# Kernel tuning notes

Hardware: AMD Instinct MI355X
Metric: run time of the kernel (lower is better)

Reference implementation:

```python
import jax, jax.numpy as jnp
import numpy as np

# Config constants (match init_kwargs)
E = 16          # n_routed_experts
G = 4           # n_groups
TOPK_G = 2      # topk_groups
K = 4           # n_activated_experts
ROUTE_SCALE = 2.5446


def setup_inputs() -> dict:
    key = jax.random.key(0)
    ks = jax.random.split(key, 9)
    T, D, H = 2048, 1024, 704
    HS = 2 * H  # shared FFN hidden = n_shared_experts * expert_hidden_dim
    sc = lambda k, shape, fan_in: (jax.random.normal(k, shape, jnp.float32)
                                   * (fan_in ** -0.5))
    return {
        "x":      jax.random.normal(ks[0], (T, D), jnp.float32),
        "gate_w": sc(ks[1], (E, D), D),
        "gate_b": jnp.zeros((E,), jnp.float32),       # V3 routing bias (init 0)
        "w1":     sc(ks[2], (E, H, D), D),            # gate proj per expert
        "w3":     sc(ks[3], (E, H, D), D),            # up proj per expert
        "w2":     sc(ks[4], (E, D, H), H),            # down proj per expert
        "ws1":    sc(ks[5], (HS, D), D),              # shared FFN gate proj
        "ws3":    sc(ks[6], (HS, D), D),              # shared FFN up proj
        "ws2":    sc(ks[7], (D, HS), HS),             # shared FFN down proj
    }


def _gate(x, gate_w, gate_b):
    """DeepSeek-V3 sigmoid gate with bias routing + group-limited masking."""
    T = x.shape[0]
    logits = x @ gate_w.T                                   # [T, E]
    scores = jax.nn.sigmoid(logits).astype(jnp.float32)     # original_scores
    routing = scores + gate_b                               # bias only affects routing
    g = routing.reshape(T, G, E // G)
    # use_bias=True -> group score = sum of top-2 routing scores in group
    group_scores = jnp.sum(jax.lax.top_k(g, 2)[0], axis=-1)     # [T, G]
    top_groups = jax.lax.top_k(group_scores, TOPK_G)[1]         # [T, TOPK_G]
    keep = jnp.any(jnp.arange(G)[None, :, None] == top_groups[:, None, :],
                   axis=-1)                                     # [T, G]
    routing = jnp.where(keep[:, :, None], g, -jnp.inf).reshape(T, E)
    idx = jax.lax.top_k(routing, K)[1]                          # [T, K]
    w = jnp.take_along_axis(scores, idx, axis=1)                # un-biased weights
    w = w / jnp.clip(jnp.sum(w, axis=-1, keepdims=True), 1e-9)  # sigmoid renorm
    w = (w * ROUTE_SCALE).astype(x.dtype)
    return w, idx


def reference(x, gate_w, gate_b, w1, w3, w2, ws1, ws3, ws2):
    T, D = x.shape
    weights, idx = _gate(x, gate_w, gate_b)                 # [T,K], [T,K]
    # Dense dispatch/combine matrix: combine[t, e] = gate weight (0 if unrouted)
    combine = jnp.zeros((T, E), x.dtype).at[
        jnp.arange(T)[:, None], idx].add(weights)           # [T, E]
    # Routed experts: SwiGLU per expert, grouped GEMMs
    hg = jnp.einsum('td,ehd->eth', x, w1)                   # [E, T, H]
    hu = jnp.einsum('td,ehd->eth', x, w3)                   # [E, T, H]
    eo = jnp.einsum('eth,edh->etd', jax.nn.silu(hg) * hu, w2)  # [E, T, D]
    y_routed = jnp.einsum('etd,te->td', eo, combine)        # [T, D]
    # Shared experts (always active SwiGLU)
    y_shared = (jax.nn.silu(x @ ws1.T) * (x @ ws3.T)) @ ws2.T
    return y_routed + y_shared
```

## Files before the change

kernel.cpp:

```cpp
#include <hip/hip_runtime.h>
#include <hip/hip_bf16.h>
#include <math.h>

typedef __attribute__((ext_vector_type(4))) float   f32x4;
typedef __attribute__((ext_vector_type(8))) short   short8;
typedef __attribute__((ext_vector_type(8))) __bf16  bf16x8;

union SB8 { short8 s; bf16x8 b; };

__device__ __forceinline__ short f2bf(float f) {
  union { float f; unsigned u; } v; v.f = f;
  unsigned r = v.u + 0x7fffu + ((v.u >> 16) & 1u);
  return (short)(r >> 16);
}

__device__ __forceinline__ short8 cvt8(f32x4 a, f32x4 b) {
  short8 r;
  r[0] = f2bf(a[0]); r[1] = f2bf(a[1]); r[2] = f2bf(a[2]); r[3] = f2bf(a[3]);
  r[4] = f2bf(b[0]); r[5] = f2bf(b[1]); r[6] = f2bf(b[2]); r[7] = f2bf(b[3]);
  return r;
}

__device__ __forceinline__ void ldsload16(const short* g, short* l) {
  __builtin_amdgcn_global_load_lds(
      (const __attribute__((address_space(1))) unsigned int*)g,
      (__attribute__((address_space(3))) unsigned int*)l, 16, 0, 0);
}

#define TT   2048
#define DD   1024
#define HH   704
#define HSS  1408
#define EE   16
#define CAP  2048
#define CSTR 32
#define XSZ  2097152ULL
#define GATE_BLOCKS 512
#define XCVT_BLOCKS 256

__global__ __launch_bounds__(256)
void gate_cvt(const float* __restrict__ x, short* __restrict__ xb,
              const float* __restrict__ gw, const float* __restrict__ gb,
              int* __restrict__ counts, int* __restrict__ tok,
              float* __restrict__ wgt, int* __restrict__ eslot)
{
  if (blockIdx.x >= GATE_BLOCKS) {
    const int tid = threadIdx.x;
    const size_t base = (size_t)(blockIdx.x - GATE_BLOCKS) * 8192;
    f32x4 va[8];
    #pragma unroll
    for (int k = 0; k < 4; k++) {
      va[2 * k]     = *(const f32x4*)(x + base + (size_t)k * 2048 + tid * 8);
      va[2 * k + 1] = *(const f32x4*)(x + base + (size_t)k * 2048 + tid * 8 + 4);
    }
    #pragma unroll
    for (int k = 0; k < 4; k++)
      *(short8*)(xb + base + (size_t)k * 2048 + tid * 8) = cvt8(va[2 * k], va[2 * k + 1]);
    return;
  }

  const int lane = threadIdx.x & 63;
  const int wid  = threadIdx.x >> 6;
  const int t    = blockIdx.x * 4 + wid;
  const int e    = lane & 15;
  const int p    = lane >> 4;

  const float* xp = x + (size_t)t * DD + p * 256;
  const float* gp = gw + (size_t)e * DD + p * 256;

  double a0 = 0.0, a1 = 0.0, a2 = 0.0, a3 = 0.0;
  #pragma unroll 8
  for (int i = 0; i < 64; i++) {
    f32x4 xa = *(const f32x4*)(xp + i * 4);
    f32x4 ga = *(const f32x4*)(gp + i * 4);
    a0 += (double)xa[0] * (double)ga[0];
    a1 += (double)xa[1] * (double)ga[1];
    a2 += (double)xa[2] * (double)ga[2];
    a3 += (double)xa[3] * (double)ga[3];
  }
  double acc = (a0 + a1) + (a2 + a3);
  acc += __shfl_xor(acc, 16);
  acc += __shfl_xor(acc, 32);
  float accf = (float)acc;

  float lf[EE], sc[EE], r[EE];
  #pragma unroll
  for (int j = 0; j < EE; j++) lf[j] = __shfl(accf, j);
  #pragma unroll
  for (int j = 0; j < EE; j++) {
    sc[j] = 1.f / (1.f + expf(-lf[j]));
    r[j] = sc[j] + gb[j];
  }
  float gs[4];
  #pragma unroll
  for (int g = 0; g < 4; g++) {
    float m1 = -1e30f, m2 = -1e30f;
    #pragma unroll
    for (int j = 0; j < 4; j++) {
      float v = r[g * 4 + j];
      if (v > m1) { m2 = m1; m1 = v; }
      else if (v > m2) { m2 = v; }
    }
    gs[g] = m1 + m2;
  }
  int g1 = 0, g2 = -1; float b1 = -1e30f, b2 = -1e30f;
  #pragma unroll
  for (int g = 0; g < 4; g++) {
    if (gs[g] > b1) { b2 = b1; g2 = g1; b1 = gs[g]; g1 = g; }
    else if (gs[g] > b2) { b2 = gs[g]; g2 = g; }
  }
  int idx[4]; float wv[4]; float wsum = 0.f;
  unsigned used = 0;
  #pragma unroll
  for (int k = 0; k < 4; k++) {
    float best = -1e30f; int bi = 0;
    #pragma unroll
    for (int j = 0; j < EE; j++) {
      int g = j >> 2;
      bool keep = (g == g1) || (g == g2);
      if (keep && !((used >> j) & 1) && r[j] > best) { best = r[j]; bi = j; }
    }
    used |= 1u << bi; idx[k] = bi; wv[k] = sc[bi]; wsum += sc[bi];
  }
  float div = wsum < 1e-9f ? 1e-9f : wsum;
  if (lane < 4) {
    float w = wv[lane] / div * 2.5446f;
    int slot = atomicAdd(&counts[idx[lane] * CSTR], 1);
    tok[idx[lane] * CAP + slot] = t;
    wgt[idx[lane] * CAP + slot] = w;
    eslot[t * 4 + lane] = (idx[lane] << 16) | slot;
  }
}

#define PIPE_VM_WAIT() do { \
    asm volatile("s_waitcnt vmcnt(0)" ::: "memory"); \
    __builtin_amdgcn_sched_barrier(0); \
    __builtin_amdgcn_s_barrier(); \
    __builtin_amdgcn_sched_barrier(0); } while (0)
#define PIPE_LGKM_BAR() do { \
    asm volatile("s_waitcnt lgkmcnt(0)" ::: "memory"); \
    __builtin_amdgcn_sched_barrier(0); \
    __builtin_amdgcn_s_barrier(); \
    __builtin_amdgcn_sched_barrier(0); } while (0)

__global__ __launch_bounds__(512, 2)
void gemm1_merged(const short* __restrict__ xb,
                  const float* __restrict__ w1f, const float* __restrict__ w3f,
                  const float* __restrict__ ws1f, const float* __restrict__ ws3f,
                  short* __restrict__ act_r, short* __restrict__ act_s,
                  const int* __restrict__ counts, const int* __restrict__ tok)
{
  const int F = blockIdx.x + 11 * (blockIdx.y + 16 * blockIdx.z);
  const int r8 = F & 7, rank = F >> 3;
  int z, Mt, Ntc;
  if (rank < 352) {
    z = r8 + 8 * (rank / 176);
    const int p = rank % 176;
    Mt = p / 11; Ntc = p % 11;
  } else {
    z = 16;
    const int p = (rank - 352) * 8 + r8;
    Mt = p / 22; Ntc = p % 22;
  }

  const bool routed = (z < EE);
  int cnt, N, rowbase = 0;
  const float *W1, *W3;
  short* act;
  if (routed) {
    cnt = counts[z * CSTR];
    if (Mt * 128 >= cnt) return;
    int rb = 0;
    for (int i = 0; i < z; i++) rb += counts[i * CSTR];
    rowbase = rb;
    N = HH;
    W1 = w1f + (size_t)z * HH * DD;
    W3 = w3f + (size_t)z * HH * DD;
    act = act_r;
  } else {
    cnt = TT; N = HSS; W1 = ws1f; W3 = ws3f; act = act_s;
  }
  const int NtB = Ntc * 64;

  __shared__ __align__(16) short lA [2][128 * 64];
  __shared__ __align__(16) short lB1[2][64 * 64];
  __shared__ __align__(16) short lB3[2][64 * 64];

  const int tid = threadIdx.x, lane = tid & 63, wv = tid >> 6;
  const int srow = lane >> 3, schunk = lane & 7, scg = schunk ^ srow;

  const short* pa[2];
  #pragma unroll
  for (int i = 0; i < 2; i++) {
    const int g = wv * 2 + i;
    int arow = Mt * 128 + g * 8 + srow;
    if (routed) {
      int slot = arow < cnt ? arow : cnt - 1;
      arow = tok[z * CAP + slot];
    }
    pa[i] = xb + (size_t)arow * DD + scg * 8;
  }
  const float *pb1f, *pb3f;
  {
    const int brow = NtB + wv * 8 + srow;
    pb1f = W1 + (size_t)brow * DD + scg * 8;
    pb3f = W3 + (size_t)brow * DD + scg * 8;
  }

  f32x4 acc1[4], acc3[4];
  #pragma unroll
  for (int i = 0; i < 4; i++) { acc1[i] = (f32x4)0.f; acc3[i] = (f32x4)0.f; }
  f32x4 rb1[2], rb3[2];

  const int q = lane >> 4, r7 = lane & 7, hi = (lane & 15) >> 3;
  const int wc = wv & 3, mh = wv >> 2;
  const int wofs = wv * 512 + srow * 64 + schunk * 8;

#define STAGE1_ISSUE(c, kk) do { \
    ldsload16(pa[0] + (kk), &lA[c][(wv * 2 + 0) * 512]); \
    ldsload16(pa[1] + (kk), &lA[c][(wv * 2 + 1) * 512]); \
    rb1[0] = *(const f32x4*)(pb1f + (kk)); \
    rb1[1] = *(const f32x4*)(pb1f + (kk) + 4); \
    rb3[0] = *(const f32x4*)(pb3f + (kk)); \
    rb3[1] = *(const f32x4*)(pb3f + (kk) + 4); } while (0)

#define STAGE1_WRITE(c) do { \
    *(short8*)(&lB1[c][wofs]) = cvt8(rb1[0], rb1[1]); \
    *(short8*)(&lB3[c][wofs]) = cvt8(rb3[0], rb3[1]); } while (0)

#define GEMM1_BODY(c) do { \
    _Pragma("unroll") for (int kc = 0; kc < 2; kc++) { \
      const int cx = (kc * 4 + q) ^ r7; \
      SB8 b1f, b3f; \
      b1f.s = *(const short8*)(&lB1[c][((wc * 2 + hi) * 64 + r7 * 8 + cx) * 8]); \
      b3f.s = *(const short8*)(&lB3[c][((wc * 2 + hi) * 64 + r7 * 8 + cx) * 8]); \
      _Pragma("unroll") for (int mt = 0; mt < 4; mt++) { \
        SB8 af; af.s = *(const short8*)(&lA[c][((2 * (mh * 4 + mt) + hi) * 64 + r7 * 8 + cx) * 8]); \
        acc1[mt] = __builtin_amdgcn_mfma_f32_16x16x32_bf16(af.b, b1f.b, acc1[mt], 0, 0, 0); \
        acc3[mt] = __builtin_amdgcn_mfma_f32_16x16x32_bf16(af.b, b3f.b, acc3[mt], 0, 0, 0); \
      } } } while (0)

  STAGE1_ISSUE(0, 0);
  asm volatile("s_waitcnt vmcnt(0)" ::: "memory");
  __builtin_amdgcn_sched_barrier(0);
  STAGE1_WRITE(0);
  PIPE_LGKM_BAR();
  int cur = 0;
  for (int kk = 64; kk < DD; kk += 64) {
    STAGE1_ISSUE(cur ^ 1, kk);
    GEMM1_BODY(cur);
    PIPE_VM_WAIT();
    STAGE1_WRITE(cur ^ 1);
    PIPE_LGKM_BAR();
    cur ^= 1;
  }
  GEMM1_BODY(cur);

  const int quad = lane >> 4, lcol = lane & 15;
  const int col = NtB + wc * 16 + lcol;
  #pragma unroll
  for (int mt = 0; mt < 4; mt++) {
    #pragma unroll
    for (int rg = 0; rg < 4; rg++) {
      const int r = Mt * 128 + (mh * 4 + mt) * 16 + quad * 4 + rg;
      if (r < cnt) {
        float g = acc1[mt][rg], u = acc3[mt][rg];
        float a = g / (1.f + __expf(-g)) * u;
        act[(size_t)(rowbase + r) * N + col] = f2bf(a);
      }
    }
  }
#undef STAGE1_ISSUE
#undef STAGE1_WRITE
#undef GEMM1_BODY
}

__global__ __launch_bounds__(512, 2)
void gemm2_merged(const short* __restrict__ act_r, const short* __restrict__ act_s,
                  const float* __restrict__ w2f, const float* __restrict__ ws2f,
                  float* __restrict__ y, float* __restrict__ outr,
                  const int* __restrict__ counts, const float* __restrict__ wgt)
{
  const int F = blockIdx.x + 8 * (blockIdx.y + 16 * blockIdx.z);
  const int r8 = F & 7, rank = F >> 3;
  int z, Mt, Nt;
  if (rank < 256) {
    z = r8 + 8 * (rank >> 7);
    const int p = rank & 127;
    Mt = p >> 3; Nt = p & 7;
  } else {
    z = 16;
    const int p = (rank - 256) * 8 + r8;
    Mt = p >> 3; Nt = p & 7;
  }

  const bool routed = (z < EE);

  int cnt, Kd, rowbase = 0;
  const short* A;
  const float* W;
  if (routed) {
    cnt = counts[z * CSTR];
    if (Mt * 128 >= cnt) return;
    int rb = 0;
    for (int i = 0; i < z; i++) rb += counts[i * CSTR];
    rowbase = rb;
    Kd = HH;
    A = act_r + (size_t)rowbase * HH;
    W = w2f + (size_t)z * DD * HH;
  } else {
    cnt = TT; Kd = HSS; A = act_s; W = ws2f;
  }

  __shared__ __align__(16) short lA[2][128 * 64];
  __shared__ __align__(16) short lB[2][128 * 64];

  const int tid = threadIdx.x, lane = tid & 63, wv = tid >> 6;
  const int srow = lane >> 3, schunk = lane & 7, scg = schunk ^ srow;

  const short* pa[2]; const float* pbf[2];
  #pragma unroll
  for (int i = 0; i < 2; i++) {
    const int g = wv * 2 + i;
    int arow = Mt * 128 + g * 8 + srow;
    if (arow >= cnt) arow = cnt - 1;
    pa[i] = A + (size_t)arow * Kd + scg * 8;
    const int brow = Nt * 128 + g * 8 + srow;
    pbf[i] = W + (size_t)brow * Kd + scg * 8;
  }

  f32x4 acc[4][2];
  #pragma unroll
  for (int i = 0; i < 4; i++) { acc[i][0] = (f32x4)0.f; acc[i][1] = (f32x4)0.f; }
  f32x4 rbw[4];

  const int q = lane >> 4, r7 = lane & 7, hi = (lane & 15) >> 3;
  const int wc = wv & 3, mh = wv >> 2;
  const int wofs0 = (wv * 2 + 0) * 512 + srow * 64 + schunk * 8;
  const int wofs1 = (wv * 2 + 1) * 512 + srow * 64 + schunk * 8;

#define STAGE2_ISSUE(c, kk) do { \
    ldsload16(pa[0] + (kk), &lA[c][(wv * 2 + 0) * 512]); \
    ldsload16(pa[1] + (kk), &lA[c][(wv * 2 + 1) * 512]); \
    rbw[0] = *(const f32x4*)(pbf[0] + (kk)); \
    rbw[1] = *(const f32x4*)(pbf[0] + (kk) + 4); \
    rbw[2] = *(const f32x4*)(pbf[1] + (kk)); \
    rbw[3] = *(const f32x4*)(pbf[1] + (kk) + 4); } while (0)

#define STAGE2_WRITE(c) do { \
    *(short8*)(&lB[c][wofs0]) = cvt8(rbw[0], rbw[1]); \
    *(short8*)(&lB[c][wofs1]) = cvt8(rbw[2], rbw[3]); } while (0)

#define GEMM2_BODY(c) do { \
    _Pragma("unroll") for (int kc = 0; kc < 2; kc++) { \
      const int cx = (kc * 4 + q) ^ r7; \
      SB8 bf[2]; \
      _Pragma("unroll") for (int ntl = 0; ntl < 2; ntl++) { \
        const int a16 = ((wc * 2 + ntl) * 2 + hi) * 64 + r7 * 8 + cx; \
        bf[ntl].s = *(const short8*)(&lB[c][a16 * 8]); \
      } \
      _Pragma("unroll") for (int mt = 0; mt < 4; mt++) { \
        const int a16 = (2 * (mh * 4 + mt) + hi) * 64 + r7 * 8 + cx; \
        SB8 af; af.s = *(const short8*)(&lA[c][a16 * 8]); \
        acc[mt][0] = __builtin_amdgcn_mfma_f32_16x16x32_bf16(af.b, bf[0].b, acc[mt][0], 0, 0, 0); \
        acc[mt][1] = __builtin_amdgcn_mfma_f32_16x16x32_bf16(af.b, bf[1].b, acc[mt][1], 0, 0, 0); \
      } } } while (0)

  STAGE2_ISSUE(0, 0);
  asm volatile("s_waitcnt vmcnt(0)" ::: "memory");
  __builtin_amdgcn_sched_barrier(0);
  STAGE2_WRITE(0);
  PIPE_LGKM_BAR();
  int cur = 0;
  for (int kk = 64; kk < Kd; kk += 64) {
    STAGE2_ISSUE(cur ^ 1, kk);
    GEMM2_BODY(cur);
    PIPE_VM_WAIT();
    STAGE2_WRITE(cur ^ 1);
    PIPE_LGKM_BAR();
    cur ^= 1;
  }
  GEMM2_BODY(cur);

  const int quad = lane >> 4, lcol = lane & 15;
  #pragma unroll
  for (int mt = 0; mt < 4; mt++) {
    #pragma unroll
    for (int ntl = 0; ntl < 2; ntl++) {
      const int col = Nt * 128 + (wc * 2 + ntl) * 16 + lcol;
      #pragma unroll
      for (int rg = 0; rg < 4; rg++) {
        const int slot = Mt * 128 + (mh * 4 + mt) * 16 + quad * 4 + rg;
        const float v = acc[mt][ntl][rg];
        if (routed) {
          if (slot < cnt) {
            const float w = wgt[z * CAP + slot];
            outr[(size_t)(rowbase + slot) * DD + col] = w * v;
          }
        } else {
          y[(size_t)slot * DD + col] = v;
        }
      }
    }
  }
#undef STAGE2_ISSUE
#undef STAGE2_WRITE
#undef GEMM2_BODY
}

__global__ __launch_bounds__(256)
void combine_kernel(float* __restrict__ y, const float* __restrict__ outr,
                    const int* __restrict__ eslot, const int* __restrict__ counts)
{
  const int t = blockIdx.x;
  const int d = threadIdx.x * 4;

  int offs[EE];
  int s = 0;
  #pragma unroll
  for (int i = 0; i < EE; i++) { offs[i] = s; s += counts[i * CSTR]; }

  f32x4 accv = *(f32x4*)(y + (size_t)t * DD + d);
  #pragma unroll
  for (int k = 0; k < 4; k++) {
    const int es = eslot[t * 4 + k];
    const int row = offs[es >> 16] + (es & 0xFFFF);
    accv += *(const f32x4*)(outr + (size_t)row * DD + d);
  }
  *(f32x4*)(y + (size_t)t * DD + d) = accv;
}

extern "C" void kernel_launch(void* const* d_in, const int* in_sizes, int n_in,
                              void* d_out, int out_size, void* d_ws, size_t ws_size,
                              hipStream_t stream) {
  const float* x      = (const float*)d_in[0];
  const float* gate_w = (const float*)d_in[1];
  const float* gate_b = (const float*)d_in[2];
  const float* w1     = (const float*)d_in[3];
  const float* w3     = (const float*)d_in[4];
  const float* w2     = (const float*)d_in[5];
  const float* ws1    = (const float*)d_in[6];
  const float* ws3    = (const float*)d_in[7];
  const float* ws2    = (const float*)d_in[8];
  float* y = (float*)d_out;

  char* ws = (char*)d_ws;
  int*   counts = (int*)ws;
  int*   tok    = (int*)(ws + 2048);
  float* wgt    = (float*)(ws + 2048 + (size_t)EE * CAP * 4);
  int*   eslot  = (int*)(ws + 2048 + (size_t)EE * CAP * 8);
  short* xb     = (short*)(ws + 2048 + (size_t)EE * CAP * 8 + (size_t)TT * 16);
  short* act_r  = xb + XSZ;
  short* act_s  = act_r + (size_t)8192 * HH;
  float* outr   = (float*)(act_s + (size_t)TT * HSS);

  (void)hipMemsetAsync(counts, 0, EE * CSTR * sizeof(int), stream);

  gate_cvt<<<GATE_BLOCKS + XCVT_BLOCKS, 256, 0, stream>>>(
      x, xb, gate_w, gate_b, counts, tok, wgt, eslot);

  gemm1_merged<<<dim3(11, TT / 128, EE + 2), 512, 0, stream>>>(
      xb, w1, w3, ws1, ws3, act_r, act_s, counts, tok);

  gemm2_merged<<<dim3(DD / 128, TT / 128, EE + 1), 512, 0, stream>>>(
      act_r, act_s, w2, ws2, y, outr, counts, wgt);

  combine_kernel<<<TT, 256, 0, stream>>>(y, outr, eslot, counts);
}
```

Measured before the change: 347.8 us.

## Pre-convert gate/up weights to bf16 and scatter outputs with atomics

The conversion kernel now turns w1, w3, ws1 and ws3 to bf16 in one bulk pass alongside x. The first GEMM can then stream all operands with direct global-to-LDS loads, using a vmcnt-based double-buffer wait in place of the register convert-and-store path. The second GEMM atomically adds weighted results straight into a zeroed y, which removes the outr buffer and the combine kernel. The cost is an extra full read and write of the weights each call, many float atomics, and a summation order that is no longer fixed.

```diff
diff --git a/kernel.cpp b/kernel.cpp
--- a/kernel.cpp
+++ b/kernel.cpp
@@ -34,28 +34,48 @@
 #define EE   16
 #define CAP  2048
 #define CSTR 32
-#define XSZ  2097152ULL
+
+#define O1  2097152ULL
+#define O2  13631488ULL
+#define O3  25165824ULL
+#define WS1END 26607616ULL
+#define CVTA_TOTAL 28049408ULL
+#define CVTA_BLOCKS 3424
 #define GATE_BLOCKS 512
-#define XCVT_BLOCKS 256
 
 __global__ __launch_bounds__(256)
-void gate_cvt(const float* __restrict__ x, short* __restrict__ xb,
+void gate_cvt(const float* __restrict__ x,  const float* __restrict__ w1,
+              const float* __restrict__ w3, const float* __restrict__ s1,
+              const float* __restrict__ s3, short* __restrict__ dst,
               const float* __restrict__ gw, const float* __restrict__ gb,
               int* __restrict__ counts, int* __restrict__ tok,
-              float* __restrict__ wgt, int* __restrict__ eslot)
+              float* __restrict__ wgt)
 {
   if (blockIdx.x >= GATE_BLOCKS) {
     const int tid = threadIdx.x;
     const size_t base = (size_t)(blockIdx.x - GATE_BLOCKS) * 8192;
+    const float* sp[4]; short* dp[4];
+    #pragma unroll
+    for (int k = 0; k < 4; k++) {
+      const size_t sb = base + (size_t)k * 2048;
+      const float* src;
+      if      (sb < O1)     src = x  + sb;
+      else if (sb < O2)     src = w1 + (sb - O1);
+      else if (sb < O3)     src = w3 + (sb - O2);
+      else if (sb < WS1END) src = s1 + (sb - O3);
+      else                  src = s3 + (sb - WS1END);
+      sp[k] = src + tid * 8;
+      dp[k] = dst + sb + tid * 8;
+    }
     f32x4 va[8];
     #pragma unroll
     for (int k = 0; k < 4; k++) {
-      va[2 * k]     = *(const f32x4*)(x + base + (size_t)k * 2048 + tid * 8);
-      va[2 * k + 1] = *(const f32x4*)(x + base + (size_t)k * 2048 + tid * 8 + 4);
+      va[2 * k]     = *(const f32x4*)(sp[k]);
+      va[2 * k + 1] = *(const f32x4*)(sp[k] + 4);
     }
     #pragma unroll
     for (int k = 0; k < 4; k++)
-      *(short8*)(xb + base + (size_t)k * 2048 + tid * 8) = cvt8(va[2 * k], va[2 * k + 1]);
+      *(short8*)(dp[k]) = cvt8(va[2 * k], va[2 * k + 1]);
     return;
   }
 
@@ -128,10 +148,22 @@
     int slot = atomicAdd(&counts[idx[lane] * CSTR], 1);
     tok[idx[lane] * CAP + slot] = t;
     wgt[idx[lane] * CAP + slot] = w;
-    eslot[t * 4 + lane] = (idx[lane] << 16) | slot;
-  }
-}
-
+  }
+}
+
+#define WAIT_PREV_TILE()  do { \
+    asm volatile("s_waitcnt vmcnt(4)" ::: "memory"); \
+    __builtin_amdgcn_sched_barrier(0); \
+    __builtin_amdgcn_s_barrier(); \
+    __builtin_amdgcn_sched_barrier(0); } while (0)
+#define WAIT_LAST_TILE()  do { \
+    asm volatile("s_waitcnt vmcnt(0)" ::: "memory"); \
+    __builtin_amdgcn_sched_barrier(0); \
+    __builtin_amdgcn_s_barrier(); \
+    __builtin_amdgcn_sched_barrier(0); } while (0)
+#define END_TILE_BARRIER() do { \
+    __builtin_amdgcn_sched_barrier(0); \
+    __builtin_amdgcn_s_barrier(); } while (0)
 #define PIPE_VM_WAIT() do { \
     asm volatile("s_waitcnt vmcnt(0)" ::: "memory"); \
     __builtin_amdgcn_sched_barrier(0); \
@@ -144,11 +176,11 @@
     __builtin_amdgcn_sched_barrier(0); } while (0)
 
 __global__ __launch_bounds__(512, 2)
-void gemm1_merged(const short* __restrict__ xb,
-                  const float* __restrict__ w1f, const float* __restrict__ w3f,
-                  const float* __restrict__ ws1f, const float* __restrict__ ws3f,
-                  short* __restrict__ act_r, short* __restrict__ act_s,
-                  const int* __restrict__ counts, const int* __restrict__ tok)
+void gemm1_merged(const short* __restrict__ xb, const short* __restrict__ w1b,
+                  const short* __restrict__ w3b, const short* __restrict__ ws1b,
+                  const short* __restrict__ ws3b, short* __restrict__ act_r,
+                  short* __restrict__ act_s, const int* __restrict__ counts,
+                  const int* __restrict__ tok)
 {
   const int F = blockIdx.x + 11 * (blockIdx.y + 16 * blockIdx.z);
   const int r8 = F & 7, rank = F >> 3;
@@ -165,7 +197,7 @@
 
   const bool routed = (z < EE);
   int cnt, N, rowbase = 0;
-  const float *W1, *W3;
+  const short *W1, *W3;
   short* act;
   if (routed) {
     cnt = counts[z * CSTR];
@@ -174,11 +206,11 @@
     for (int i = 0; i < z; i++) rb += counts[i * CSTR];
     rowbase = rb;
     N = HH;
-    W1 = w1f + (size_t)z * HH * DD;
-    W3 = w3f + (size_t)z * HH * DD;
+    W1 = w1b + (size_t)z * HH * DD;
+    W3 = w3b + (size_t)z * HH * DD;
     act = act_r;
   } else {
-    cnt = TT; N = HSS; W1 = ws1f; W3 = ws3f; act = act_s;
+    cnt = TT; N = HSS; W1 = ws1b; W3 = ws3b; act = act_s;
   }
   const int NtB = Ntc * 64;
 
@@ -200,33 +232,25 @@
     }
     pa[i] = xb + (size_t)arow * DD + scg * 8;
   }
-  const float *pb1f, *pb3f;
+  const short *pb1, *pb3;
   {
     const int brow = NtB + wv * 8 + srow;
-    pb1f = W1 + (size_t)brow * DD + scg * 8;
-    pb3f = W3 + (size_t)brow * DD + scg * 8;
+    pb1 = W1 + (size_t)brow * DD + scg * 8;
+    pb3 = W3 + (size_t)brow * DD + scg * 8;
   }
 
   f32x4 acc1[4], acc3[4];
   #pragma unroll
   for (int i = 0; i < 4; i++) { acc1[i] = (f32x4)0.f; acc3[i] = (f32x4)0.f; }
-  f32x4 rb1[2], rb3[2];
 
   const int q = lane >> 4, r7 = lane & 7, hi = (lane & 15) >> 3;
   const int wc = wv & 3, mh = wv >> 2;
-  const int wofs = wv * 512 + srow * 64 + schunk * 8;
-
-#define STAGE1_ISSUE(c, kk) do { \
-    ldsload16(pa[0] + (kk), &lA[c][(wv * 2 + 0) * 512]); \
-    ldsload16(pa[1] + (kk), &lA[c][(wv * 2 + 1) * 512]); \
-    rb1[0] = *(const f32x4*)(pb1f + (kk)); \
-    rb1[1] = *(const f32x4*)(pb1f + (kk) + 4); \
-    rb3[0] = *(const f32x4*)(pb3f + (kk)); \
-    rb3[1] = *(const f32x4*)(pb3f + (kk) + 4); } while (0)
-
-#define STAGE1_WRITE(c) do { \
-    *(short8*)(&lB1[c][wofs]) = cvt8(rb1[0], rb1[1]); \
-    *(short8*)(&lB3[c][wofs]) = cvt8(rb3[0], rb3[1]); } while (0)
+
+#define STAGE1(c, kk) do { \
+    ldsload16(pa[0] + (kk), &lA [c][(wv * 2 + 0) * 512]); \
+    ldsload16(pa[1] + (kk), &lA [c][(wv * 2 + 1) * 512]); \
+    ldsload16(pb1  + (kk),  &lB1[c][wv * 512]); \
+    ldsload16(pb3  + (kk),  &lB3[c][wv * 512]); } while (0)
 
 #define GEMM1_BODY(c) do { \
     _Pragma("unroll") for (int kc = 0; kc < 2; kc++) { \
@@ -240,20 +264,16 @@
         acc3[mt] = __builtin_amdgcn_mfma_f32_16x16x32_bf16(af.b, b3f.b, acc3[mt], 0, 0, 0); \
       } } } while (0)
 
-  STAGE1_ISSUE(0, 0);
-  asm volatile("s_waitcnt vmcnt(0)" ::: "memory");
-  __builtin_amdgcn_sched_barrier(0);
-  STAGE1_WRITE(0);
-  PIPE_LGKM_BAR();
+  STAGE1(0, 0);
   int cur = 0;
   for (int kk = 64; kk < DD; kk += 64) {
-    STAGE1_ISSUE(cur ^ 1, kk);
+    STAGE1(cur ^ 1, kk);
+    WAIT_PREV_TILE();
     GEMM1_BODY(cur);
-    PIPE_VM_WAIT();
-    STAGE1_WRITE(cur ^ 1);
-    PIPE_LGKM_BAR();
+    END_TILE_BARRIER();
     cur ^= 1;
   }
+  WAIT_LAST_TILE();
   GEMM1_BODY(cur);
 
   const int quad = lane >> 4, lcol = lane & 15;
@@ -270,16 +290,16 @@
       }
     }
   }
-#undef STAGE1_ISSUE
-#undef STAGE1_WRITE
+#undef STAGE1
 #undef GEMM1_BODY
 }
 
 __global__ __launch_bounds__(512, 2)
 void gemm2_merged(const short* __restrict__ act_r, const short* __restrict__ act_s,
                   const float* __restrict__ w2f, const float* __restrict__ ws2f,
-                  float* __restrict__ y, float* __restrict__ outr,
-                  const int* __restrict__ counts, const float* __restrict__ wgt)
+                  float* __restrict__ y,
+                  const int* __restrict__ counts, const float* __restrict__ wgt,
+                  const int* __restrict__ tok)
 {
   const int F = blockIdx.x + 8 * (blockIdx.y + 16 * blockIdx.z);
   const int r8 = F & 7, rank = F >> 3;
@@ -395,10 +415,11 @@
         if (routed) {
           if (slot < cnt) {
             const float w = wgt[z * CAP + slot];
-            outr[(size_t)(rowbase + slot) * DD + col] = w * v;
+            const int t = tok[z * CAP + slot];
+            atomicAdd(&y[(size_t)t * DD + col], w * v);
           }
         } else {
-          y[(size_t)slot * DD + col] = v;
+          atomicAdd(&y[(size_t)slot * DD + col], v);
         }
       }
     }
@@ -406,28 +427,6 @@
 #undef STAGE2_ISSUE
 #undef STAGE2_WRITE
 #undef GEMM2_BODY
-}
-
-__global__ __launch_bounds__(256)
-void combine_kernel(float* __restrict__ y, const float* __restrict__ outr,
-                    const int* __restrict__ eslot, const int* __restrict__ counts)
-{
-  const int t = blockIdx.x;
-  const int d = threadIdx.x * 4;
-
-  int offs[EE];
-  int s = 0;
-  #pragma unroll
-  for (int i = 0; i < EE; i++) { offs[i] = s; s += counts[i * CSTR]; }
-
-  f32x4 accv = *(f32x4*)(y + (size_t)t * DD + d);
-  #pragma unroll
-  for (int k = 0; k < 4; k++) {
-    const int es = eslot[t * 4 + k];
-    const int row = offs[es >> 16] + (es & 0xFFFF);
-    accv += *(const f32x4*)(outr + (size_t)row * DD + d);
-  }
-  *(f32x4*)(y + (size_t)t * DD + d) = accv;
 }
 
 extern "C" void kernel_launch(void* const* d_in, const int* in_sizes, int n_in,
@@ -448,22 +447,25 @@
   int*   counts = (int*)ws;
   int*   tok    = (int*)(ws + 2048);
   float* wgt    = (float*)(ws + 2048 + (size_t)EE * CAP * 4);
-  int*   eslot  = (int*)(ws + 2048 + (size_t)EE * CAP * 8);
-  short* xb     = (short*)(ws + 2048 + (size_t)EE * CAP * 8 + (size_t)TT * 16);
-  short* act_r  = xb + XSZ;
-  short* act_s  = act_r + (size_t)8192 * HH;
-  float* outr   = (float*)(act_s + (size_t)TT * HSS);
+  short* bf     = (short*)(ws + 2048 + (size_t)EE * CAP * 8);
+  short* xb   = bf;
+  short* w1b  = bf + O1;
+  short* w3b  = bf + O2;
+  short* ws1b = bf + O3;
+  short* ws3b = bf + WS1END;
+  short* act_r = bf + CVTA_TOTAL;
+  short* act_s = act_r + (size_t)8192 * HH;
 
   (void)hipMemsetAsync(counts, 0, EE * CSTR * sizeof(int), stream);
-
-  gate_cvt<<<GATE_BLOCKS + XCVT_BLOCKS, 256, 0, stream>>>(
-      x, xb, gate_w, gate_b, counts, tok, wgt, eslot);
+  (void)hipMemsetAsync(y, 0, (size_t)TT * DD * sizeof(float), stream);
+
+  gate_cvt<<<GATE_BLOCKS + CVTA_BLOCKS, 256, 0, stream>>>(
+      x, w1, w3, ws1, ws3, bf,
+      gate_w, gate_b, counts, tok, wgt);
 
   gemm1_merged<<<dim3(11, TT / 128, EE + 2), 512, 0, stream>>>(
-      xb, w1, w3, ws1, ws3, act_r, act_s, counts, tok);
+      xb, w1b, w3b, ws1b, ws3b, act_r, act_s, counts, tok);
 
   gemm2_merged<<<dim3(DD / 128, TT / 128, EE + 1), 512, 0, stream>>>(
-      act_r, act_s, w2, ws2, y, outr, counts, wgt);
-
-  combine_kernel<<<TT, 256, 0, stream>>>(y, outr, eslot, counts);
-}
+      act_r, act_s, w2, ws2, y, counts, wgt, tok);
+}
```

Measured after the change: 331.3 us. 1.05x faster.
